# Optimization experiments

Hardware: AMD Instinct MI355X
Metric: run time of the kernel (lower is better)

The kernel has to match this reference:

```python
import jax, jax.numpy as jnp
import numpy as np
import math

D_MODEL = 1024
N_HEAD = 16
HEAD_DIM = D_MODEL // N_HEAD
SEQ_LEN = 512
INIT_SIZE = 1568  # from RelativeSinusoidalPositionalEmbedding default


def _rel_pos_embedding(seq_len, embedding_dim):
    # Replicates RelativeSinusoidalPositionalEmbedding with init_size=1568
    num_embeddings = INIT_SIZE + 1  # 1569
    half_dim = embedding_dim // 2
    scale = math.log(10000.0) / (half_dim - 1)
    freqs = np.exp(np.arange(half_dim, dtype=np.float32) * -scale)
    pos = np.arange(-(num_embeddings // 2), num_embeddings // 2, dtype=np.float32)  # [-785, 784)
    emb = pos[:, None] * freqs[None, :]
    weights = np.concatenate([np.sin(emb), np.cos(emb)], axis=1).astype(np.float32)  # (1569, d)
    weights[0, :] = 0.0  # padding_idx
    origin_shift = num_embeddings // 2 + 1  # 785
    positions = np.arange(-seq_len, seq_len) + origin_shift
    embed = weights[positions]  # (2*seq_len, d)
    return jnp.asarray(embed.T)  # (d, 2*seq_len), matching .T in __init__


def setup_inputs() -> dict:
    key = jax.random.key(0)
    k1, k2, k3, k4, k5 = jax.random.split(key, 5)
    x = jax.random.normal(k1, (8, SEQ_LEN, D_MODEL), dtype=jnp.float32)
    prev = jax.random.normal(k2, (8, N_HEAD, SEQ_LEN, SEQ_LEN), dtype=jnp.float32)
    # Linear(d_model, 3*d_model, bias=False): store as (d_model, 3*d_model) for x @ W
    Wqkv = jax.random.normal(k3, (D_MODEL, 3 * D_MODEL), dtype=jnp.float32) / math.sqrt(D_MODEL)
    r_r_bias = jax.random.normal(k4, (1, N_HEAD, 1, HEAD_DIM), dtype=jnp.float32) * 0.02
    r_w_bias = jax.random.normal(k5, (1, N_HEAD, 1, HEAD_DIM), dtype=jnp.float32) * 0.02
    rel_pos = _rel_pos_embedding(SEQ_LEN, HEAD_DIM)  # (head_dim, 2*seq_len)
    return {"x": x, "prev": prev, "Wqkv": Wqkv, "r_r_bias": r_r_bias,
            "r_w_bias": r_w_bias, "rel_pos": rel_pos, "skip_op": 1}


def _shift(BD, seq_len):
    # BD: (b, h, L, 2L) -> (b, h, L, L) via Transformer-XL pad/reshape trick
    b, h, L, two_L = BD.shape
    BD = jnp.pad(BD, ((0, 0), (0, 0), (0, 0), (0, 1)))        # (b,h,L,2L+1)
    BD = BD.reshape(b, h, -1, L)                               # (b,h,2L+1,L)
    BD = BD[:, :, :-1].reshape(b, h, L, -1)                    # (b,h,L,2L)
    return BD[:, :, :, seq_len:]                               # (b,h,L,L)


def reference(x, prev, Wqkv, r_r_bias, r_w_bias, rel_pos, skip_op):
    b, L, d = x.shape
    qkv = x @ Wqkv                                             # (b,L,3d)
    q, k, v = jnp.split(qkv, 3, axis=-1)
    q = q.reshape(b, L, N_HEAD, HEAD_DIM).transpose(0, 2, 1, 3)  # (b,h,L,hd)
    k = k.reshape(b, L, N_HEAD, HEAD_DIM).transpose(0, 2, 1, 3)
    v = v.reshape(b, L, N_HEAD, HEAD_DIM).transpose(0, 2, 1, 3)

    AC = jnp.einsum('bhqd,bhkd->bhqk', q + r_r_bias, k)
    BD = jnp.einsum('bhqd,dp->bhqp', q + r_w_bias, rel_pos)    # (b,h,L,2L)
    BD = _shift(BD, SEQ_LEN)
    E = jnp.einsum('bhkd,dp->bhkp', k, rel_pos)
    E = _shift(E, SEQ_LEN).transpose(0, 1, 3, 2)
    attn_score = (AC + BD + E) / math.sqrt(HEAD_DIM)
    if skip_op:
        attn_score = attn_score + prev
    prev_out = attn_score
    attn = jax.nn.softmax(attn_score, axis=-1)
    out = jnp.einsum('bhqk,bhkd->bhqd', attn, v)
    out = out.transpose(0, 2, 1, 3).reshape(b, L, d)
    return out, prev_out
```

## Files before the change

### kernel.cpp

```cpp
#include <hip/hip_runtime.h>
#include <hip/hip_bf16.h>
#include <math.h>

namespace {
constexpr int Bn = 8;
constexpr int Hn = 16;
constexpr int Ln = 512;
constexpr int HD = 64;
constexpr int DM = 1024;
constexpr int TL = 1024;
constexpr size_t QS  = (size_t)Bn * Hn * Ln * HD;
constexpr size_t FSz = (size_t)Hn * Ln * Ln;
constexpr size_t WN  = (size_t)DM * 3 * DM;
}

typedef __bf16 bf16x8 __attribute__((ext_vector_type(8)));
typedef float f32x4 __attribute__((ext_vector_type(4)));

typedef __attribute__((address_space(1))) void as1_void_t;
typedef __attribute__((address_space(3))) void as3_void_t;

__device__ __forceinline__ void gload_lds16(const void* g, void* l) {
  __builtin_amdgcn_global_load_lds((as1_void_t*)g, (as3_void_t*)l, 16, 0, 0);
}

__device__ __forceinline__ unsigned short f2bf(float f) {
  unsigned int u = __float_as_uint(f);
  u += 0x7fffu + ((u >> 16) & 1u);
  return (unsigned short)(u >> 16);
}
__device__ __forceinline__ float bf2f(unsigned short h) {
  return __uint_as_float(((unsigned int)h) << 16);
}

__global__ __launch_bounds__(256) void conv_x(const float* __restrict__ x,
                                              unsigned short* __restrict__ xh,
                                              unsigned short* __restrict__ xl) {
  size_t i = ((size_t)blockIdx.x * 256 + threadIdx.x) * 4;
  float4 v = *(const float4*)(x + i);
  unsigned short h0 = f2bf(v.x), h1 = f2bf(v.y), h2 = f2bf(v.z), h3 = f2bf(v.w);
  ushort4 hv = make_ushort4(h0, h1, h2, h3);
  ushort4 lv = make_ushort4(f2bf(v.x - bf2f(h0)), f2bf(v.y - bf2f(h1)),
                            f2bf(v.z - bf2f(h2)), f2bf(v.w - bf2f(h3)));
  *(ushort4*)(xh + i) = hv;
  *(ushort4*)(xl + i) = lv;
}

__global__ __launch_bounds__(256) void conv_w(const float* __restrict__ W,
                                              unsigned short* __restrict__ wh,
                                              unsigned short* __restrict__ wl) {
  __shared__ unsigned short Th[64][72];
  __shared__ unsigned short Tl[64][72];
  const int t = threadIdx.x;
  const int n0 = blockIdx.x * 64;
  const int k0 = blockIdx.y * 64;
#pragma unroll
  for (int i = 0; i < 4; ++i) {
    int row = i * 16 + (t >> 4);
    int col = (t & 15) * 4;
    float4 v = *(const float4*)(W + (size_t)(k0 + row) * 3072 + n0 + col);
    unsigned short h;
    h = f2bf(v.x); Th[row][col + 0] = h; Tl[row][col + 0] = f2bf(v.x - bf2f(h));
    h = f2bf(v.y); Th[row][col + 1] = h; Tl[row][col + 1] = f2bf(v.y - bf2f(h));
    h = f2bf(v.z); Th[row][col + 2] = h; Tl[row][col + 2] = f2bf(v.z - bf2f(h));
    h = f2bf(v.w); Th[row][col + 3] = h; Tl[row][col + 3] = f2bf(v.w - bf2f(h));
  }
  __syncthreads();
  const int rn = t & 63, qq = t >> 6;
  unsigned int hw[8], lw[8];
#pragma unroll
  for (int j = 0; j < 8; ++j) {
    unsigned short a = Th[qq * 16 + 2 * j][rn], b = Th[qq * 16 + 2 * j + 1][rn];
    hw[j] = (unsigned int)a | ((unsigned int)b << 16);
    unsigned short c = Tl[qq * 16 + 2 * j][rn], d = Tl[qq * 16 + 2 * j + 1][rn];
    lw[j] = (unsigned int)c | ((unsigned int)d << 16);
  }
  size_t o = (size_t)(n0 + rn) * 1024 + k0 + qq * 16;
  *(uint4*)(wh + o)     = make_uint4(hw[0], hw[1], hw[2], hw[3]);
  *(uint4*)(wh + o + 8) = make_uint4(hw[4], hw[5], hw[6], hw[7]);
  *(uint4*)(wl + o)     = make_uint4(lw[0], lw[1], lw[2], lw[3]);
  *(uint4*)(wl + o + 8) = make_uint4(lw[4], lw[5], lw[6], lw[7]);
}

__global__ __launch_bounds__(256, 2) void qkv_mfma(const unsigned short* __restrict__ xh,
                                                   const unsigned short* __restrict__ xl,
                                                   const unsigned short* __restrict__ wh,
                                                   const unsigned short* __restrict__ wl,
                                                   const float* __restrict__ rrb,
                                                   unsigned short* __restrict__ qrh,
                                                   unsigned short* __restrict__ qrl,
                                                   unsigned short* __restrict__ kharr,
                                                   unsigned short* __restrict__ klarr,
                                                   unsigned short* __restrict__ vTh,
                                                   unsigned short* __restrict__ vTl) {
  __shared__ alignas(16) unsigned short Ah[128 * 32];
  __shared__ alignas(16) unsigned short Al[128 * 32];
  __shared__ alignas(16) unsigned short Bh[128 * 32];
  __shared__ alignas(16) unsigned short Bl[128 * 32];
  const int t = threadIdx.x;
  const int lane = t & 63;
  const int w = t >> 6;
  const int m0 = blockIdx.y * 128;
  const int n0 = blockIdx.x * 128;
  const int wr = w >> 1, wc = w & 1;
  const int l16 = lane & 15, s = lane >> 4;

  const unsigned short* gsrc = (w == 0) ? xh : (w == 1) ? xl : (w == 2) ? wh : wl;
  unsigned short* lbase = (w == 0) ? Ah : (w == 1) ? Al : (w == 2) ? Bh : Bl;
  const int rbase = (w < 2) ? m0 : n0;
  const int srow = lane >> 2, sc = lane & 3;

  int aoff[4], boff[4];
#pragma unroll
  for (int f = 0; f < 4; ++f) {
    int Rm = wr * 64 + f * 16 + l16;
    aoff[f] = Rm * 64 + ((s ^ ((Rm >> 1) & 3)) << 4);
    int Rn = wc * 64 + f * 16 + l16;
    boff[f] = Rn * 64 + ((s ^ ((Rn >> 1) & 3)) << 4);
  }

  f32x4 acc[4][4];
#pragma unroll
  for (int i = 0; i < 4; ++i)
#pragma unroll
    for (int j = 0; j < 4; ++j) acc[i][j] = (f32x4){0.f, 0.f, 0.f, 0.f};

  const char* Ahc = (const char*)Ah;
  const char* Alc = (const char*)Al;
  const char* Bhc = (const char*)Bh;
  const char* Blc = (const char*)Bl;

  for (int k0 = 0; k0 < 1024; k0 += 32) {
#pragma unroll
    for (int u = 0; u < 8; ++u) {
      int row = u * 16 + srow;
      int chunk = sc ^ ((row >> 1) & 3);
      gload_lds16(gsrc + (size_t)(rbase + row) * 1024 + k0 + chunk * 8,
                  lbase + u * 512);
    }
    __syncthreads();

    bf16x8 a_h[4], a_l[4], b_h[4], b_l[4];
#pragma unroll
    for (int f = 0; f < 4; ++f) {
      a_h[f] = *(const bf16x8*)(Ahc + aoff[f]);
      b_h[f] = *(const bf16x8*)(Bhc + boff[f]);
    }
#pragma unroll
    for (int i = 0; i < 4; ++i)
#pragma unroll
      for (int j = 0; j < 4; ++j)
        acc[i][j] = __builtin_amdgcn_mfma_f32_16x16x32_bf16(a_h[i], b_h[j], acc[i][j], 0, 0, 0);
#pragma unroll
    for (int f = 0; f < 4; ++f) b_l[f] = *(const bf16x8*)(Blc + boff[f]);
#pragma unroll
    for (int i = 0; i < 4; ++i)
#pragma unroll
      for (int j = 0; j < 4; ++j)
        acc[i][j] = __builtin_amdgcn_mfma_f32_16x16x32_bf16(a_h[i], b_l[j], acc[i][j], 0, 0, 0);
#pragma unroll
    for (int f = 0; f < 4; ++f) a_l[f] = *(const bf16x8*)(Alc + aoff[f]);
#pragma unroll
    for (int i = 0; i < 4; ++i)
#pragma unroll
      for (int j = 0; j < 4; ++j)
        acc[i][j] = __builtin_amdgcn_mfma_f32_16x16x32_bf16(a_l[i], b_h[j], acc[i][j], 0, 0, 0);
    __syncthreads();
  }

  const int part = n0 >> 10;
  const int nb = n0 & 1023;
#pragma unroll
  for (int i = 0; i < 4; ++i) {
#pragma unroll
    for (int j = 0; j < 4; ++j) {
      const int n = nb + wc * 64 + j * 16 + l16;
      const int h = n >> 6, d = n & 63;
      const int mb = m0 + wr * 64 + i * 16 + (lane >> 4) * 4;
      const int bb = mb >> 9, lb = mb & 511;
      const size_t rowbase = ((size_t)(bb * Hn + h) * Ln + lb) << 6;
      if (part == 0) {
        const float rr = rrb[h * HD + d];
#pragma unroll
        for (int r = 0; r < 4; ++r) {
          const float qv = acc[i][j][r] + rr;
          const size_t qi = rowbase + ((size_t)r << 6) + d;
          const unsigned short hh = f2bf(qv);
          qrh[qi] = hh;
          qrl[qi] = f2bf(qv - bf2f(hh));
        }
      } else if (part == 1) {
#pragma unroll
        for (int r = 0; r < 4; ++r) {
          const float v = acc[i][j][r];
          const size_t qi = rowbase + ((size_t)r << 6) + d;
          const unsigned short hh = f2bf(v);
          kharr[qi] = hh;
          klarr[qi] = f2bf(v - bf2f(hh));
        }
      } else {
        ushort4 hv, lv;
        unsigned short* hp = &hv.x;
        unsigned short* lp = &lv.x;
#pragma unroll
        for (int r = 0; r < 4; ++r) {
          const float v = acc[i][j][r];
          const unsigned short hh = f2bf(v);
          hp[r] = hh;
          lp[r] = f2bf(v - bf2f(hh));
        }
        const size_t vi = ((size_t)(bb * Hn + h) * HD + d) * Ln + lb;
        *(ushort4*)(vTh + vi) = hv;
        *(ushort4*)(vTl + vi) = lv;
      }
    }
  }
}

__global__ __launch_bounds__(256) void fg_gemm(const unsigned short* __restrict__ qrh,
                                               const unsigned short* __restrict__ qrl,
                                               const unsigned short* __restrict__ kharr,
                                               const unsigned short* __restrict__ klarr,
                                               const float* __restrict__ rrb,
                                               const float* __restrict__ rwb,
                                               const float* __restrict__ R,
                                               float* __restrict__ Fs,
                                               float* __restrict__ Gs,
                                               int b) {
  const int m0 = blockIdx.y * 64;
  const int n0 = blockIdx.x * 64;
  if (m0 + n0 + 126 < 512 || m0 + n0 >= 1024) return;

  __shared__ float As[64][68];
  __shared__ float Rs[64][68];
  const int t = threadIdx.x;
  const int h = blockIdx.z >> 1;
  const int which = blockIdx.z & 1;
  const size_t abase = (size_t)(b * Hn + h) * Ln * HD;
  const unsigned short* Ahp = (which == 0 ? qrh : kharr) + abase;
  const unsigned short* Alp = (which == 0 ? qrl : klarr) + abase;

#pragma unroll
  for (int i = 0; i < 4; ++i) {
    int idx = t + i * 256;
    int r = idx >> 4;
    int c4 = (idx & 15) * 4;
    ushort4 h4 = *(const ushort4*)(Ahp + (size_t)(m0 + r) * HD + c4);
    ushort4 l4 = *(const ushort4*)(Alp + (size_t)(m0 + r) * HD + c4);
    float vx = bf2f(h4.x) + bf2f(l4.x);
    float vy = bf2f(h4.y) + bf2f(l4.y);
    float vz = bf2f(h4.z) + bf2f(l4.z);
    float vw = bf2f(h4.w) + bf2f(l4.w);
    if (which == 0) {
      float4 rr = *(const float4*)(rrb + h * HD + c4);
      float4 rw = *(const float4*)(rwb + h * HD + c4);
      vx += rw.x - rr.x; vy += rw.y - rr.y;
      vz += rw.z - rr.z; vw += rw.w - rr.w;
    }
    As[c4 + 0][r] = vx; As[c4 + 1][r] = vy;
    As[c4 + 2][r] = vz; As[c4 + 3][r] = vw;
    *(float4*)(&Rs[r][c4]) = *(const float4*)(R + (size_t)r * TL + n0 + c4);
  }
  __syncthreads();
  const int tr = t >> 4, tc = t & 15;
  float acc[4][4];
#pragma unroll
  for (int i = 0; i < 4; ++i)
#pragma unroll
    for (int j = 0; j < 4; ++j) acc[i][j] = 0.f;
#pragma unroll 16
  for (int kk = 0; kk < 64; ++kk) {
    float a[4], bb[4];
    *(float4*)(a)  = *(const float4*)(&As[kk][tr * 4]);
    *(float4*)(bb) = *(const float4*)(&Rs[kk][tc * 4]);
#pragma unroll
    for (int i = 0; i < 4; ++i)
#pragma unroll
      for (int j = 0; j < 4; ++j) acc[i][j] = fmaf(a[i], bb[j], acc[i][j]);
  }
  if (which == 0) {
    float* O = Fs + (size_t)h * Ln * Ln;
#pragma unroll
    for (int i = 0; i < 4; ++i) {
      const int q = m0 + tr * 4 + i;
#pragma unroll
      for (int jj = 0; jj < 4; ++jj) {
        const int p = n0 + tc * 4 + jj;
        const int j = p + q - 512;
        if ((unsigned)j < 512u) O[((size_t)q << 9) + j] = acc[i][jj];
      }
    }
  } else {
    float* O = Gs + (size_t)h * Ln * Ln;
#pragma unroll
    for (int i = 0; i < 4; ++i) {
      const int jrow = m0 + tr * 4 + i;
#pragma unroll
      for (int jj = 0; jj < 4; ++jj) {
        const int p = n0 + tc * 4 + jj;
        const int q = p + jrow - 512;
        if ((unsigned)q < 512u) O[((size_t)q << 9) + jrow] = acc[i][jj];
      }
    }
  }
}

__global__ __launch_bounds__(256) void attn_mfma(const unsigned short* __restrict__ qrh,
                                                 const unsigned short* __restrict__ qrl,
                                                 const unsigned short* __restrict__ kharr,
                                                 const unsigned short* __restrict__ klarr,
                                                 const unsigned short* __restrict__ vTh,
                                                 const unsigned short* __restrict__ vTl,
                                                 const float* __restrict__ Fs,
                                                 const float* __restrict__ Gs,
                                                 const float* __restrict__ prev,
                                                 const int* __restrict__ skip,
                                                 float* __restrict__ out,
                                                 float* __restrict__ pout,
                                                 int b) {
  __shared__ alignas(16) unsigned short PhL[4][16 * 64];
  __shared__ alignas(16) unsigned short PlL[4][16 * 64];
  __shared__ float Om[4][16][65];
  __shared__ float mw[4][16];
  __shared__ float lw[4][16];

  const int t = threadIdx.x;
  const int w = t >> 6;
  const int lane = t & 63;
  const int s = lane >> 4, l16 = lane & 15;
  const int h = blockIdx.y;
  const int q0 = blockIdx.x * 16;
  const size_t bh = (size_t)(b * Hn + h);
  const float pf = (skip[0] != 0) ? 1.f : 0.f;

  bf16x8 aqh[2], aql[2];
#pragma unroll
  for (int kd = 0; kd < 2; ++kd) {
    const size_t a = ((bh * Ln + q0 + l16) << 6) + kd * 32 + s * 8;
    aqh[kd] = *(const bf16x8*)(qrh + a);
    aql[kd] = *(const bf16x8*)(qrl + a);
  }

  float m_run[4] = {-INFINITY, -INFINITY, -INFINITY, -INFINITY};
  float l_run[4] = {0.f, 0.f, 0.f, 0.f};
  f32x4 O[4];
#pragma unroll
  for (int fo = 0; fo < 4; ++fo) O[fo] = (f32x4){0.f, 0.f, 0.f, 0.f};

  const int qrow = q0 + s * 4;
  unsigned short* PhW = &PhL[w][0];
  unsigned short* PlW = &PlL[w][0];

#pragma unroll
  for (int it = 0; it < 2; ++it) {
    const int j0 = (w * 2 + it) * 64;

    f32x4 S[4];
#pragma unroll
    for (int fi = 0; fi < 4; ++fi) S[fi] = (f32x4){0.f, 0.f, 0.f, 0.f};
#pragma unroll
    for (int kd = 0; kd < 2; ++kd) {
#pragma unroll
      for (int fi = 0; fi < 4; ++fi) {
        const size_t ka = ((bh * Ln + j0 + fi * 16 + l16) << 6) + kd * 32 + s * 8;
        const bf16x8 bkh = *(const bf16x8*)(kharr + ka);
        const bf16x8 bkl = *(const bf16x8*)(klarr + ka);
        S[fi] = __builtin_amdgcn_mfma_f32_16x16x32_bf16(aqh[kd], bkh, S[fi], 0, 0, 0);
        S[fi] = __builtin_amdgcn_mfma_f32_16x16x32_bf16(aqh[kd], bkl, S[fi], 0, 0, 0);
        S[fi] = __builtin_amdgcn_mfma_f32_16x16x32_bf16(aql[kd], bkh, S[fi], 0, 0, 0);
      }
    }

    float sc[4][4];
    float mx[4] = {-INFINITY, -INFINITY, -INFINITY, -INFINITY};
#pragma unroll
    for (int fi = 0; fi < 4; ++fi) {
      const int j = j0 + fi * 16 + l16;
#pragma unroll
      for (int r = 0; r < 4; ++r) {
        const int q = qrow + r;
        const size_t fb = (((size_t)h * Ln + q) << 9) + j;
        const size_t pb = ((bh * Ln + q) << 9) + j;
        const float v = (S[fi][r] + Fs[fb] + Gs[fb]) * 0.125f + pf * prev[pb];
        pout[pb] = v;
        sc[fi][r] = v;
        mx[r] = fmaxf(mx[r], v);
      }
    }

    float al[4];
#pragma unroll
    for (int r = 0; r < 4; ++r) {
      float m = mx[r];
      m = fmaxf(m, __shfl_xor(m, 1));
      m = fmaxf(m, __shfl_xor(m, 2));
      m = fmaxf(m, __shfl_xor(m, 4));
      m = fmaxf(m, __shfl_xor(m, 8));
      const float mn = fmaxf(m_run[r], m);
      al[r] = __expf(m_run[r] - mn);
      m_run[r] = mn;
    }

    float sum[4] = {0.f, 0.f, 0.f, 0.f};
#pragma unroll
    for (int fi = 0; fi < 4; ++fi) {
      const int jloc = fi * 16 + l16;
      const int chunk = jloc >> 3, sub = jloc & 7;
#pragma unroll
      for (int r = 0; r < 4; ++r) {
        const float p = __expf(sc[fi][r] - m_run[r]);
        sum[r] += p;
        const unsigned short ph = f2bf(p);
        const unsigned short pl = f2bf(p - bf2f(ph));
        const int qloc = s * 4 + r;
        const int idx = (qloc << 6) + ((chunk ^ (qloc & 7)) << 3) + sub;
        PhW[idx] = ph;
        PlW[idx] = pl;
      }
    }
#pragma unroll
    for (int r = 0; r < 4; ++r) {
      float sm = sum[r];
      sm += __shfl_xor(sm, 1);
      sm += __shfl_xor(sm, 2);
      sm += __shfl_xor(sm, 4);
      sm += __shfl_xor(sm, 8);
      l_run[r] = l_run[r] * al[r] + sm;
    }

#pragma unroll
    for (int fo = 0; fo < 4; ++fo)
#pragma unroll
      for (int r = 0; r < 4; ++r) O[fo][r] *= al[r];

#pragma unroll
    for (int kj = 0; kj < 2; ++kj) {
      const int raddr = (l16 << 6) + (((kj * 4 + s) ^ (l16 & 7)) << 3);
      const bf16x8 pah = *(const bf16x8*)(PhW + raddr);
      const bf16x8 pal = *(const bf16x8*)(PlW + raddr);
#pragma unroll
      for (int fo = 0; fo < 4; ++fo) {
        const size_t va = ((bh << 6) + fo * 16 + l16) * (size_t)Ln + j0 + kj * 32 + s * 8;
        const bf16x8 vbh = *(const bf16x8*)(vTh + va);
        const bf16x8 vbl = *(const bf16x8*)(vTl + va);
        O[fo] = __builtin_amdgcn_mfma_f32_16x16x32_bf16(pah, vbh, O[fo], 0, 0, 0);
        O[fo] = __builtin_amdgcn_mfma_f32_16x16x32_bf16(pah, vbl, O[fo], 0, 0, 0);
        O[fo] = __builtin_amdgcn_mfma_f32_16x16x32_bf16(pal, vbh, O[fo], 0, 0, 0);
      }
    }
  }

  if (l16 == 0) {
#pragma unroll
    for (int r = 0; r < 4; ++r) {
      mw[w][s * 4 + r] = m_run[r];
      lw[w][s * 4 + r] = l_run[r];
    }
  }
  __syncthreads();

  float fw[4];
#pragma unroll
  for (int r = 0; r < 4; ++r) {
    const int ql_ = s * 4 + r;
    const float g = fmaxf(fmaxf(mw[0][ql_], mw[1][ql_]), fmaxf(mw[2][ql_], mw[3][ql_]));
    fw[r] = __expf(m_run[r] - g);
  }
#pragma unroll
  for (int fo = 0; fo < 4; ++fo)
#pragma unroll
    for (int r = 0; r < 4; ++r)
      Om[w][s * 4 + r][fo * 16 + l16] = O[fo][r] * fw[r];
  __syncthreads();

  {
    const int q = t >> 4;
    const int d0 = (t & 15) * 4;
    const float g = fmaxf(fmaxf(mw[0][q], mw[1][q]), fmaxf(mw[2][q], mw[3][q]));
    const float lt = lw[0][q] * __expf(mw[0][q] - g) + lw[1][q] * __expf(mw[1][q] - g) +
                     lw[2][q] * __expf(mw[2][q] - g) + lw[3][q] * __expf(mw[3][q] - g);
    const float inv = 1.0f / lt;
    float4 o4;
    o4.x = (Om[0][q][d0 + 0] + Om[1][q][d0 + 0] + Om[2][q][d0 + 0] + Om[3][q][d0 + 0]) * inv;
    o4.y = (Om[0][q][d0 + 1] + Om[1][q][d0 + 1] + Om[2][q][d0 + 1] + Om[3][q][d0 + 1]) * inv;
    o4.z = (Om[0][q][d0 + 2] + Om[1][q][d0 + 2] + Om[2][q][d0 + 2] + Om[3][q][d0 + 2]) * inv;
    o4.w = (Om[0][q][d0 + 3] + Om[1][q][d0 + 3] + Om[2][q][d0 + 3] + Om[3][q][d0 + 3]) * inv;
    *(float4*)(out + ((size_t)b * Ln + q0 + q) * DM + h * HD + d0) = o4;
  }
}

extern "C" void kernel_launch(void* const* d_in, const int* in_sizes, int n_in,
                              void* d_out, int out_size, void* d_ws, size_t ws_size,
                              hipStream_t stream) {
  const float* x    = (const float*)d_in[0];
  const float* prev = (const float*)d_in[1];
  const float* W    = (const float*)d_in[2];
  const float* rrb  = (const float*)d_in[3];
  const float* rwb  = (const float*)d_in[4];
  const float* R    = (const float*)d_in[5];
  const int*   skip = (const int*)d_in[6];

  float* out  = (float*)d_out;
  float* pout = out + (size_t)Bn * Ln * DM;

  float* ws = (float*)d_ws;
  unsigned short* qrh = (unsigned short*)ws;
  unsigned short* qrl = qrh + QS;
  unsigned short* kh  = qrl + QS;
  unsigned short* kl  = kh + QS;
  unsigned short* vTh = kl + QS;
  unsigned short* vTl = vTh + QS;
  float* Farr = ws + 3 * QS;
  float* Garr = Farr + FSz;

  unsigned short* xh = (unsigned short*)Farr;
  unsigned short* xl = xh + QS;
  unsigned short* wwh = xl + QS;
  unsigned short* wwl = wwh + WN;

  conv_x<<<dim3(4096), 256, 0, stream>>>(x, xh, xl);
  conv_w<<<dim3(48, 16), 256, 0, stream>>>(W, wwh, wwl);
  qkv_mfma<<<dim3(24, 32), 256, 0, stream>>>(xh, xl, wwh, wwl, rrb,
                                             qrh, qrl, kh, kl, vTh, vTl);
  for (int b = 0; b < Bn; ++b) {
    fg_gemm<<<dim3(TL / 64, Ln / 64, Hn * 2), 256, 0, stream>>>(qrh, qrl, kh, kl, rrb, rwb, R,
                                                                Farr, Garr, b);
    attn_mfma<<<dim3(Ln / 16, Hn), 256, 0, stream>>>(qrh, qrl, kh, kl, vTh, vTl,
                                                     Farr, Garr, prev, skip, out, pout, b);
  }
}
```

Baseline: 977.5 us.

## Batch two batches per launch, transpose G store via LDS, drop P low split, add setprio

Processes two batch elements per fg_gemm/attn_mfma launch with double-sized F/G scratch, halving launch count and raising occupancy per launch. The transposed G write now goes through shared memory so each thread writes contiguous row segments instead of strided scattered stores. The low-order bf16 part of the softmax probabilities is dropped, removing one MFMA and LDS traffic per PV step at some accuracy cost, and s_setprio wraps MFMA sections. Workspace for F/G now needs twice the size, which may overlap other buffers if the workspace layout was tight.

```diff
diff --git a/kernel.cpp b/kernel.cpp
--- a/kernel.cpp
+++ b/kernel.cpp
@@ -224,9 +224,8 @@
                                                const float* __restrict__ rrb,
                                                const float* __restrict__ rwb,
                                                const float* __restrict__ R,
-                                               float* __restrict__ Fs,
-                                               float* __restrict__ Gs,
-                                               int b) {
+                                               float* __restrict__ FG,
+                                               int bpair) {
   const int m0 = blockIdx.y * 64;
   const int n0 = blockIdx.x * 64;
   if (m0 + n0 + 126 < 512 || m0 + n0 >= 1024) return;
@@ -234,8 +233,12 @@
   __shared__ float As[64][68];
   __shared__ float Rs[64][68];
   const int t = threadIdx.x;
-  const int h = blockIdx.z >> 1;
-  const int which = blockIdx.z & 1;
+  const int zz = blockIdx.z;
+  const int b = bpair * 2 + (zz >> 5);
+  const int h = (zz & 31) >> 1;
+  const int which = zz & 1;
+  float* Fs = FG + (size_t)(b & 1) * 2 * FSz;
+  float* Gs = Fs + FSz;
   const size_t abase = (size_t)(b * Hn + h) * Ln * HD;
   const unsigned short* Ahp = (which == 0 ? qrh : kharr) + abase;
   const unsigned short* Alp = (which == 0 ? qrl : klarr) + abase;
@@ -291,15 +294,28 @@
       }
     }
   } else {
+    float* T = &As[0][0];
+    __syncthreads();
+#pragma unroll
+    for (int i = 0; i < 4; ++i)
+#pragma unroll
+      for (int jj = 0; jj < 4; ++jj)
+        T[(tr * 4 + i) * 65 + tc * 4 + jj] = acc[i][jj];
+    __syncthreads();
     float* O = Gs + (size_t)h * Ln * Ln;
-#pragma unroll
-    for (int i = 0; i < 4; ++i) {
-      const int jrow = m0 + tr * 4 + i;
-#pragma unroll
-      for (int jj = 0; jj < 4; ++jj) {
-        const int p = n0 + tc * 4 + jj;
-        const int q = p + jrow - 512;
-        if ((unsigned)q < 512u) O[((size_t)q << 9) + jrow] = acc[i][jj];
+    const int u = t >> 1;
+    const int half = t & 1;
+    if (u <= 126) {
+      const int qv = n0 + m0 - 512 + u;
+      if ((unsigned)qv < 512u) {
+        const int lo = (u > 63) ? (u - 63) : 0;
+        const int hi = (u < 63) ? u : 63;
+        const int beg = lo + half * 32;
+        const int end = (hi < beg + 31) ? hi : (beg + 31);
+        float* Orow = O + ((size_t)qv << 9) + m0;
+        for (int mr = beg; mr <= end; ++mr) {
+          Orow[mr] = T[mr * 65 + (u - mr)];
+        }
       }
     }
   }
@@ -311,15 +327,13 @@
                                                  const unsigned short* __restrict__ klarr,
                                                  const unsigned short* __restrict__ vTh,
                                                  const unsigned short* __restrict__ vTl,
-                                                 const float* __restrict__ Fs,
-                                                 const float* __restrict__ Gs,
+                                                 const float* __restrict__ FG,
                                                  const float* __restrict__ prev,
                                                  const int* __restrict__ skip,
                                                  float* __restrict__ out,
                                                  float* __restrict__ pout,
-                                                 int b) {
+                                                 int bpair) {
   __shared__ alignas(16) unsigned short PhL[4][16 * 64];
-  __shared__ alignas(16) unsigned short PlL[4][16 * 64];
   __shared__ float Om[4][16][65];
   __shared__ float mw[4][16];
   __shared__ float lw[4][16];
@@ -330,8 +344,11 @@
   const int s = lane >> 4, l16 = lane & 15;
   const int h = blockIdx.y;
   const int q0 = blockIdx.x * 16;
+  const int b = bpair * 2 + blockIdx.z;
   const size_t bh = (size_t)(b * Hn + h);
   const float pf = (skip[0] != 0) ? 1.f : 0.f;
+  const float* Fs = FG + (size_t)(b & 1) * 2 * FSz;
+  const float* Gs = Fs + FSz;
 
   bf16x8 aqh[2], aql[2];
 #pragma unroll
@@ -349,7 +366,6 @@
 
   const int qrow = q0 + s * 4;
   unsigned short* PhW = &PhL[w][0];
-  unsigned short* PlW = &PlL[w][0];
 
 #pragma unroll
   for (int it = 0; it < 2; ++it) {
@@ -358,6 +374,7 @@
     f32x4 S[4];
 #pragma unroll
     for (int fi = 0; fi < 4; ++fi) S[fi] = (f32x4){0.f, 0.f, 0.f, 0.f};
+    __builtin_amdgcn_s_setprio(1);
 #pragma unroll
     for (int kd = 0; kd < 2; ++kd) {
 #pragma unroll
@@ -370,6 +387,7 @@
         S[fi] = __builtin_amdgcn_mfma_f32_16x16x32_bf16(aql[kd], bkh, S[fi], 0, 0, 0);
       }
     }
+    __builtin_amdgcn_s_setprio(0);
 
     float sc[4][4];
     float mx[4] = {-INFINITY, -INFINITY, -INFINITY, -INFINITY};
@@ -410,12 +428,9 @@
       for (int r = 0; r < 4; ++r) {
         const float p = __expf(sc[fi][r] - m_run[r]);
         sum[r] += p;
-        const unsigned short ph = f2bf(p);
-        const unsigned short pl = f2bf(p - bf2f(ph));
         const int qloc = s * 4 + r;
         const int idx = (qloc << 6) + ((chunk ^ (qloc & 7)) << 3) + sub;
-        PhW[idx] = ph;
-        PlW[idx] = pl;
+        PhW[idx] = f2bf(p);
       }
     }
 #pragma unroll
@@ -433,11 +448,11 @@
 #pragma unroll
       for (int r = 0; r < 4; ++r) O[fo][r] *= al[r];
 
+    __builtin_amdgcn_s_setprio(1);
 #pragma unroll
     for (int kj = 0; kj < 2; ++kj) {
       const int raddr = (l16 << 6) + (((kj * 4 + s) ^ (l16 & 7)) << 3);
       const bf16x8 pah = *(const bf16x8*)(PhW + raddr);
-      const bf16x8 pal = *(const bf16x8*)(PlW + raddr);
 #pragma unroll
       for (int fo = 0; fo < 4; ++fo) {
         const size_t va = ((bh << 6) + fo * 16 + l16) * (size_t)Ln + j0 + kj * 32 + s * 8;
@@ -445,9 +460,9 @@
         const bf16x8 vbl = *(const bf16x8*)(vTl + va);
         O[fo] = __builtin_amdgcn_mfma_f32_16x16x32_bf16(pah, vbh, O[fo], 0, 0, 0);
         O[fo] = __builtin_amdgcn_mfma_f32_16x16x32_bf16(pah, vbl, O[fo], 0, 0, 0);
-        O[fo] = __builtin_amdgcn_mfma_f32_16x16x32_bf16(pal, vbh, O[fo], 0, 0, 0);
-      }
-    }
+      }
+    }
+    __builtin_amdgcn_s_setprio(0);
   }
 
   if (l16 == 0) {
@@ -510,10 +525,9 @@
   unsigned short* kl  = kh + QS;
   unsigned short* vTh = kl + QS;
   unsigned short* vTl = vTh + QS;
-  float* Farr = ws + 3 * QS;
-  float* Garr = Farr + FSz;
-
-  unsigned short* xh = (unsigned short*)Farr;
+  float* FG = ws + 3 * QS;
+
+  unsigned short* xh = (unsigned short*)FG;
   unsigned short* xl = xh + QS;
   unsigned short* wwh = xl + QS;
   unsigned short* wwl = wwh + WN;
@@ -522,10 +536,10 @@
   conv_w<<<dim3(48, 16), 256, 0, stream>>>(W, wwh, wwl);
   qkv_mfma<<<dim3(24, 32), 256, 0, stream>>>(xh, xl, wwh, wwl, rrb,
                                              qrh, qrl, kh, kl, vTh, vTl);
-  for (int b = 0; b < Bn; ++b) {
-    fg_gemm<<<dim3(TL / 64, Ln / 64, Hn * 2), 256, 0, stream>>>(qrh, qrl, kh, kl, rrb, rwb, R,
-                                                                Farr, Garr, b);
-    attn_mfma<<<dim3(Ln / 16, Hn), 256, 0, stream>>>(qrh, qrl, kh, kl, vTh, vTl,
-                                                     Farr, Garr, prev, skip, out, pout, b);
-  }
-}
+  for (int bp = 0; bp < 4; ++bp) {
+    fg_gemm<<<dim3(TL / 64, Ln / 64, Hn * 2 * 2), 256, 0, stream>>>(qrh, qrl, kh, kl, rrb, rwb, R,
+                                                                    FG, bp);
+    attn_mfma<<<dim3(Ln / 16, Hn, 2), 256, 0, stream>>>(qrh, qrl, kh, kl, vTh, vTl,
+                                                        FG, prev, skip, out, pout, bp);
+  }
+}
```

New measurement: 1.014 ms. +3.7%, slower.
